# Optimization experiments

Hardware: AMD Instinct MI355X
Metric: run time of the kernel (lower is better)

The kernel has to match this reference:

```python
import jax, jax.numpy as jnp
import numpy as np

OUT_FEATURES = 4096
IN_FEATURES = 4096
NNZ = 1677722
BATCH, SEQ = 2, 2048


def setup_inputs() -> dict:
    key = jax.random.key(0)
    k1, k2, k3, k4 = jax.random.split(key, 4)
    x = jax.random.normal(k1, (BATCH, SEQ, IN_FEATURES), dtype=jnp.float32)
    data = jax.random.normal(k2, (NNZ,), dtype=jnp.float32)
    rows = jax.random.randint(k3, (NNZ,), 0, OUT_FEATURES, dtype=jnp.int32)
    cols = jax.random.randint(k4, (NNZ,), 0, IN_FEATURES, dtype=jnp.int32)
    return {"x": x, "data": data, "rows": rows, "cols": cols}


def reference(x, data, rows, cols):
    # Densify sparse weight W [out_features, in_features] from COO triples
    # (equivalent math to the CSR spmm in the original module).
    W = jnp.zeros((OUT_FEATURES, IN_FEATURES), dtype=data.dtype)
    W = W.at[rows, cols].add(data)
    # Original: (W @ x_flat.T).T reshaped -> y = x @ W^T, shape [B, S, out]
    return jnp.einsum("bsi,oi->bso", x, W)
```

## Files before the change

kernel.cpp:

```cpp
#include <hip/hip_runtime.h>
#include <stdint.h>

#define M_ROWS 4096
#define N_OUT  4096
#define K_IN   4096
#define NNZ_N  1677722
#define CAP    640

typedef __attribute__((ext_vector_type(8))) short  bf16x8_t;
typedef __attribute__((ext_vector_type(4))) float  f32x4_t;

__device__ __forceinline__ unsigned short f2bf(float f) {
    union { float f; uint32_t u; } v; v.f = f;
    uint32_t u = v.u;
    u += 0x7FFFu + ((u >> 16) & 1u);
    return (unsigned short)(u >> 16);
}

__global__ void convert_x_zero_cnt(const float4* __restrict__ x,
                                   uint4* __restrict__ xo,
                                   uint4* __restrict__ cntz) {
    int i = blockIdx.x * blockDim.x + threadIdx.x;
    if (i < 16384) {
        uint4 z; z.x = z.y = z.z = z.w = 0u;
        cntz[i] = z;
    }
    float4 a = x[2 * i], b = x[2 * i + 1];
    uint4 o;
    o.x = (uint32_t)f2bf(a.x) | ((uint32_t)f2bf(a.y) << 16);
    o.y = (uint32_t)f2bf(a.z) | ((uint32_t)f2bf(a.w) << 16);
    o.z = (uint32_t)f2bf(b.x) | ((uint32_t)f2bf(b.y) << 16);
    o.w = (uint32_t)f2bf(b.z) | ((uint32_t)f2bf(b.w) << 16);
    xo[i] = o;
}

__global__ void bin_coo(const float* __restrict__ data,
                        const int* __restrict__ rows,
                        const int* __restrict__ cols,
                        uint32_t* __restrict__ cnt,
                        uint32_t* __restrict__ bucket, int nnz) {
    int i = blockIdx.x * blockDim.x + threadIdx.x;
    if (i >= nnz) return;
    int r = rows[i];
    uint32_t slot = atomicAdd(&cnt[r << 4], 1u);
    if (slot < CAP)
        bucket[(size_t)r * CAP + slot] =
            ((uint32_t)cols[i] << 16) | (uint32_t)f2bf(data[i]);
}

__global__ __launch_bounds__(256) void accum_rows(const uint32_t* __restrict__ cnt,
                                                  const uint32_t* __restrict__ bucket,
                                                  unsigned short* __restrict__ W) {
    __shared__ float acc[K_IN];
    const int r = blockIdx.x;
    const int t = threadIdx.x;

    float4* av = (float4*)acc;
#pragma unroll
    for (int j = t; j < K_IN / 4; j += 256) av[j] = (float4){0.f, 0.f, 0.f, 0.f};
    __syncthreads();

    uint32_t n = cnt[r << 4];
    if (n > CAP) n = CAP;
    const uint32_t* b = bucket + (size_t)r * CAP;
    for (uint32_t j = t; j < n; j += 256) {
        uint32_t e = b[j];
        union { uint32_t u; float f; } v; v.u = (e & 0xFFFFu) << 16;
        atomicAdd(&acc[e >> 16], v.f);
    }
    __syncthreads();

    uint4* wv = (uint4*)(W + (size_t)r * K_IN);
#pragma unroll
    for (int j = t; j < K_IN / 8; j += 256) {
        float4 a = av[2 * j], c = av[2 * j + 1];
        uint4 o;
        o.x = (uint32_t)f2bf(a.x) | ((uint32_t)f2bf(a.y) << 16);
        o.y = (uint32_t)f2bf(a.z) | ((uint32_t)f2bf(a.w) << 16);
        o.z = (uint32_t)f2bf(c.x) | ((uint32_t)f2bf(c.y) << 16);
        o.w = (uint32_t)f2bf(c.z) | ((uint32_t)f2bf(c.w) << 16);
        wv[j] = o;
    }
}

__device__ __forceinline__ void async_ld16(const void* g, void* lds_wave_base) {
    __builtin_amdgcn_global_load_lds(
        (const __attribute__((address_space(1))) uint32_t*)g,
        (__attribute__((address_space(3))) uint32_t*)lds_wave_base,
        16, 0, 0);
}

#define STAGE_M(gbase, lbase, kt, slot) do {                                   \
    const unsigned short* g_ = (gbase) + (kt) * 64;                            \
    unsigned short*       l_ = (lbase) + (slot) * 32768;                       \
    async_ld16(g_,                  l_);                                       \
    async_ld16(g_ + 1 * 64 * K_IN,  l_ + 4096);                                \
    async_ld16(g_ + 2 * 64 * K_IN,  l_ + 8192);                                \
    async_ld16(g_ + 3 * 64 * K_IN,  l_ + 12288);                               \
} while (0)

__global__ __launch_bounds__(512, 2) void gemm_bt(const unsigned short* __restrict__ A,
                                                  const unsigned short* __restrict__ B,
                                                  float* __restrict__ C) {
    __shared__ __align__(16) unsigned short lds_[65536];

    const int t    = threadIdx.x;
    const int wave = t >> 6;
    const int lane = t & 63;
    const int wr   = wave >> 2;
    const int wc   = wave & 3;
    const int m0   = blockIdx.y * 256;
    const int n0   = blockIdx.x * 256;

    const int srow = t >> 3;
    const int sch  = ((t & 7) ^ (srow & 7)) * 8;
    const unsigned short* gA = A + (size_t)(m0 + srow) * K_IN + sch;
    const unsigned short* gB = B + (size_t)(n0 + srow) * K_IN + sch;
    unsigned short* lA = lds_ + wave * 512;
    unsigned short* lB = lds_ + 16384 + wave * 512;

    const int l15  = lane & 15;
    const int aoff = (wr * 128 + l15) * 64;
    const int boff = (wc * 64  + l15) * 64;
    const int ck0  = (((lane >> 4)    ) ^ (lane & 7)) * 8;
    const int ck1  = (((lane >> 4) | 4) ^ (lane & 7)) * 8;

    f32x4_t acc[8][4];
#pragma unroll
    for (int i = 0; i < 8; ++i)
#pragma unroll
        for (int j = 0; j < 4; ++j) acc[i][j] = (f32x4_t){0.f, 0.f, 0.f, 0.f};

    bf16x8_t af[4][2], bf0[2][2], bf1[2][2];

    STAGE_M(gA, lA, 0, 0); STAGE_M(gB, lB, 0, 0);
    STAGE_M(gA, lA, 1, 1); STAGE_M(gB, lB, 1, 1);
    asm volatile("s_waitcnt vmcnt(8)" ::: "memory");
    __builtin_amdgcn_s_barrier();

    for (int kt = 0; kt < 64; ++kt) {
        const unsigned short* pA = lds_ + (kt & 1) * 32768;
        const unsigned short* pB = pA + 16384;

#pragma unroll
        for (int im = 0; im < 4; ++im) {
            af[im][0] = *(const bf16x8_t*)(pA + aoff + im * 1024 + ck0);
            af[im][1] = *(const bf16x8_t*)(pA + aoff + im * 1024 + ck1);
        }
#pragma unroll
        for (int jn = 0; jn < 2; ++jn) {
            bf0[jn][0] = *(const bf16x8_t*)(pB + boff + jn * 1024 + ck0);
            bf0[jn][1] = *(const bf16x8_t*)(pB + boff + jn * 1024 + ck1);
        }
        __builtin_amdgcn_s_barrier();
        asm volatile("s_waitcnt lgkmcnt(0)" ::: "memory");
        __builtin_amdgcn_s_setprio(1);
#pragma unroll
        for (int im = 0; im < 4; ++im)
#pragma unroll
            for (int jn = 0; jn < 2; ++jn)
#pragma unroll
                for (int kk = 0; kk < 2; ++kk)
                    acc[im][jn] = __builtin_amdgcn_mfma_f32_16x16x32_bf16(
                        af[im][kk], bf0[jn][kk], acc[im][jn], 0, 0, 0);
        __builtin_amdgcn_s_setprio(0);
        __builtin_amdgcn_s_barrier();

#pragma unroll
        for (int jn = 0; jn < 2; ++jn) {
            bf1[jn][0] = *(const bf16x8_t*)(pB + boff + (2 + jn) * 1024 + ck0);
            bf1[jn][1] = *(const bf16x8_t*)(pB + boff + (2 + jn) * 1024 + ck1);
        }
        __builtin_amdgcn_s_barrier();
        asm volatile("s_waitcnt lgkmcnt(0)" ::: "memory");
        __builtin_amdgcn_s_setprio(1);
#pragma unroll
        for (int im = 0; im < 4; ++im)
#pragma unroll
            for (int jn = 0; jn < 2; ++jn)
#pragma unroll
                for (int kk = 0; kk < 2; ++kk)
                    acc[im][2 + jn] = __builtin_amdgcn_mfma_f32_16x16x32_bf16(
                        af[im][kk], bf1[jn][kk], acc[im][2 + jn], 0, 0, 0);
        __builtin_amdgcn_s_setprio(0);
        __builtin_amdgcn_s_barrier();

        if (kt < 62) STAGE_M(gB, lB, kt + 2, (kt & 1));
#pragma unroll
        for (int im = 0; im < 4; ++im) {
            af[im][0] = *(const bf16x8_t*)(pA + aoff + (4 + im) * 1024 + ck0);
            af[im][1] = *(const bf16x8_t*)(pA + aoff + (4 + im) * 1024 + ck1);
        }
        __builtin_amdgcn_s_barrier();
        asm volatile("s_waitcnt lgkmcnt(0)" ::: "memory");
        __builtin_amdgcn_s_setprio(1);
#pragma unroll
        for (int im = 0; im < 4; ++im)
#pragma unroll
            for (int jn = 0; jn < 2; ++jn)
#pragma unroll
                for (int kk = 0; kk < 2; ++kk)
                    acc[4 + im][jn] = __builtin_amdgcn_mfma_f32_16x16x32_bf16(
                        af[im][kk], bf0[jn][kk], acc[4 + im][jn], 0, 0, 0);
        __builtin_amdgcn_s_setprio(0);
        __builtin_amdgcn_s_barrier();

        if (kt < 62) STAGE_M(gA, lA, kt + 2, (kt & 1));
        __builtin_amdgcn_s_setprio(1);
#pragma unroll
        for (int im = 0; im < 4; ++im)
#pragma unroll
            for (int jn = 0; jn < 2; ++jn)
#pragma unroll
                for (int kk = 0; kk < 2; ++kk)
                    acc[4 + im][2 + jn] = __builtin_amdgcn_mfma_f32_16x16x32_bf16(
                        af[im][kk], bf1[jn][kk], acc[4 + im][2 + jn], 0, 0, 0);
        __builtin_amdgcn_s_setprio(0);
        if (kt < 62) {
            asm volatile("s_waitcnt vmcnt(8)" ::: "memory");
        } else {
            asm volatile("s_waitcnt vmcnt(0)" ::: "memory");
        }
        __builtin_amdgcn_s_barrier();
    }

    const int crow = m0 + wr * 128 + ((lane >> 4) << 2);
    const int ccol = n0 + wc * 64 + l15;
#pragma unroll
    for (int im = 0; im < 8; ++im)
#pragma unroll
        for (int jn = 0; jn < 4; ++jn)
#pragma unroll
            for (int r = 0; r < 4; ++r)
                C[(size_t)(crow + im * 16 + r) * N_OUT + ccol + jn * 16] =
                    acc[im][jn][r];
}

extern "C" void kernel_launch(void* const* d_in, const int* in_sizes, int n_in,
                              void* d_out, int out_size, void* d_ws, size_t ws_size,
                              hipStream_t stream) {
    const float* x    = (const float*)d_in[0];
    const float* data = (const float*)d_in[1];
    const int*   rows = (const int*)d_in[2];
    const int*   cols = (const int*)d_in[3];
    float*       out  = (float*)d_out;

    unsigned short* W_bf16 = (unsigned short*)d_ws;
    unsigned short* x_bf16 = (unsigned short*)((char*)d_ws + (32u << 20));
    uint32_t*       cnt    = (uint32_t*)((char*)d_ws + (64u << 20));
    uint32_t*       bucket = (uint32_t*)((char*)d_ws + (65u << 20));

    convert_x_zero_cnt<<<(M_ROWS * K_IN) / (8 * 256), 256, 0, stream>>>(
        (const float4*)x, (uint4*)x_bf16, (uint4*)cnt);

    bin_coo<<<(NNZ_N + 255) / 256, 256, 0, stream>>>(
        data, rows, cols, cnt, bucket, NNZ_N);

    accum_rows<<<N_OUT, 256, 0, stream>>>(cnt, bucket, W_bf16);

    dim3 grid(N_OUT / 256, M_ROWS / 256);
    gemm_bt<<<grid, 512, 0, stream>>>(x_bf16, W_bf16, out);
}
```

Baseline: 338.2 us.

## Replace global-atomic COO binning with block histogram, scan, and LDS placement

Replaces the single binning kernel, which did one global atomicAdd per nonzero on padded per-row counters, with three kernels. Each block first builds a per-chunk row histogram in shared memory, then a scan turns the histograms into per-block base offsets, and a placement pass writes entries using shared-memory atomics. The aim is to remove contention on global atomics in exchange for two extra launches, a second read of the rows array, and a histogram buffer held in global memory.

```diff
diff --git a/kernel.cpp b/kernel.cpp
--- a/kernel.cpp
+++ b/kernel.cpp
@@ -6,6 +6,8 @@
 #define K_IN   4096
 #define NNZ_N  1677722
 #define CAP    640
+#define NB     256
+#define BCHUNK 6656
 
 typedef __attribute__((ext_vector_type(8))) short  bf16x8_t;
 typedef __attribute__((ext_vector_type(4))) float  f32x4_t;
@@ -17,14 +19,8 @@
     return (unsigned short)(u >> 16);
 }
 
-__global__ void convert_x_zero_cnt(const float4* __restrict__ x,
-                                   uint4* __restrict__ xo,
-                                   uint4* __restrict__ cntz) {
+__global__ void convert_x(const float4* __restrict__ x, uint4* __restrict__ xo) {
     int i = blockIdx.x * blockDim.x + threadIdx.x;
-    if (i < 16384) {
-        uint4 z; z.x = z.y = z.z = z.w = 0u;
-        cntz[i] = z;
-    }
     float4 a = x[2 * i], b = x[2 * i + 1];
     uint4 o;
     o.x = (uint32_t)f2bf(a.x) | ((uint32_t)f2bf(a.y) << 16);
@@ -34,18 +30,65 @@
     xo[i] = o;
 }
 
-__global__ void bin_coo(const float* __restrict__ data,
-                        const int* __restrict__ rows,
-                        const int* __restrict__ cols,
-                        uint32_t* __restrict__ cnt,
-                        uint32_t* __restrict__ bucket, int nnz) {
-    int i = blockIdx.x * blockDim.x + threadIdx.x;
-    if (i >= nnz) return;
-    int r = rows[i];
-    uint32_t slot = atomicAdd(&cnt[r << 4], 1u);
-    if (slot < CAP)
-        bucket[(size_t)r * CAP + slot] =
-            ((uint32_t)cols[i] << 16) | (uint32_t)f2bf(data[i]);
+__global__ __launch_bounds__(1024) void hist_coo(const int* __restrict__ rows,
+                                                 uint32_t* __restrict__ Hist) {
+    __shared__ uint32_t h[N_OUT];
+    const int blk = blockIdx.x, t = threadIdx.x;
+    for (int j = t; j < N_OUT; j += 1024) h[j] = 0;
+    __syncthreads();
+    const int start = blk * BCHUNK;
+    const int end   = min(start + BCHUNK, NNZ_N);
+    for (int i = start + t; i < end; i += 1024)
+        atomicAdd(&h[rows[i]], 1u);
+    __syncthreads();
+    for (int j = t; j < N_OUT; j += 1024)
+        Hist[(size_t)blk * N_OUT + j] = h[j];
+}
+
+__global__ __launch_bounds__(256) void scan_hist(uint32_t* __restrict__ Hist,
+                                                 uint32_t* __restrict__ cnt) {
+    const int bin  = blockIdx.x * 4 + (threadIdx.x >> 6);
+    const int lane = threadIdx.x & 63;
+    uint32_t v[4], pre[4];
+#pragma unroll
+    for (int q = 0; q < 4; ++q)
+        v[q] = Hist[(size_t)(lane * 4 + q) * N_OUT + bin];
+    pre[0] = 0;
+#pragma unroll
+    for (int q = 1; q < 4; ++q) pre[q] = pre[q - 1] + v[q - 1];
+    uint32_t tot = pre[3] + v[3];
+    uint32_t x = tot;
+#pragma unroll
+    for (int off = 1; off < 64; off <<= 1) {
+        uint32_t y = __shfl_up(x, off);
+        if (lane >= off) x += y;
+    }
+    uint32_t excl = x - tot;
+#pragma unroll
+    for (int q = 0; q < 4; ++q)
+        Hist[(size_t)(lane * 4 + q) * N_OUT + bin] = excl + pre[q];
+    if (lane == 63) cnt[bin] = excl + tot;
+}
+
+__global__ __launch_bounds__(1024) void place_coo(const float* __restrict__ data,
+                                                  const int* __restrict__ rows,
+                                                  const int* __restrict__ cols,
+                                                  const uint32_t* __restrict__ Base,
+                                                  uint32_t* __restrict__ bucket) {
+    __shared__ uint32_t cur[N_OUT];
+    const int blk = blockIdx.x, t = threadIdx.x;
+    for (int j = t; j < N_OUT; j += 1024)
+        cur[j] = Base[(size_t)blk * N_OUT + j];
+    __syncthreads();
+    const int start = blk * BCHUNK;
+    const int end   = min(start + BCHUNK, NNZ_N);
+    for (int i = start + t; i < end; i += 1024) {
+        int r = rows[i];
+        uint32_t slot = atomicAdd(&cur[r], 1u);
+        if (slot < CAP)
+            bucket[(size_t)r * CAP + slot] =
+                ((uint32_t)cols[i] << 16) | (uint32_t)f2bf(data[i]);
+    }
 }
 
 __global__ __launch_bounds__(256) void accum_rows(const uint32_t* __restrict__ cnt,
@@ -60,7 +103,7 @@
     for (int j = t; j < K_IN / 4; j += 256) av[j] = (float4){0.f, 0.f, 0.f, 0.f};
     __syncthreads();
 
-    uint32_t n = cnt[r << 4];
+    uint32_t n = cnt[r];
     if (n > CAP) n = CAP;
     const uint32_t* b = bucket + (size_t)r * CAP;
     for (uint32_t j = t; j < n; j += 256) {
@@ -247,14 +290,18 @@
 
     unsigned short* W_bf16 = (unsigned short*)d_ws;
     unsigned short* x_bf16 = (unsigned short*)((char*)d_ws + (32u << 20));
-    uint32_t*       cnt    = (uint32_t*)((char*)d_ws + (64u << 20));
-    uint32_t*       bucket = (uint32_t*)((char*)d_ws + (65u << 20));
-
-    convert_x_zero_cnt<<<(M_ROWS * K_IN) / (8 * 256), 256, 0, stream>>>(
-        (const float4*)x, (uint4*)x_bf16, (uint4*)cnt);
-
-    bin_coo<<<(NNZ_N + 255) / 256, 256, 0, stream>>>(
-        data, rows, cols, cnt, bucket, NNZ_N);
+    uint32_t*       Hist   = (uint32_t*)((char*)d_ws + (64u << 20));
+    uint32_t*       cnt    = (uint32_t*)((char*)d_ws + (68u << 20));
+    uint32_t*       bucket = (uint32_t*)((char*)d_ws + (69u << 20));
+
+    convert_x<<<(M_ROWS * K_IN) / (8 * 256), 256, 0, stream>>>(
+        (const float4*)x, (uint4*)x_bf16);
+
+    hist_coo<<<NB, 1024, 0, stream>>>(rows, Hist);
+
+    scan_hist<<<N_OUT / 4, 256, 0, stream>>>(Hist, cnt);
+
+    place_coo<<<NB, 1024, 0, stream>>>(data, rows, cols, Hist, bucket);
 
     accum_rows<<<N_OUT, 256, 0, stream>>>(cnt, bucket, W_bf16);
 
```

After: 316.4 us. 6.4% less time.

## Replace global-atomic COO bucketing with block-local counting sort and binned accumulation

Applied to the files above, without the earlier changes.

Drops the global atomic bucketing of COO entries into fixed-capacity per-row buckets. Each of 128 blocks now counting-sorts its chunk of entries into 512 bins of 8 rows in shared memory and writes per-bin offsets. A second kernel then has each block gather its bin's segments from every chunk and accumulate 8 dense rows in 128KB of LDS before writing bf16. This removes global atomics and the silent drop of entries past the bucket cap. In exchange it uses large LDS per block, giving low occupancy, and only 128 blocks in the sort pass.

```diff
diff --git a/kernel.cpp b/kernel.cpp
--- a/kernel.cpp
+++ b/kernel.cpp
@@ -5,7 +5,9 @@
 #define N_OUT  4096
 #define K_IN   4096
 #define NNZ_N  1677722
-#define CAP    640
+#define NBLK_A 128
+#define CHUNK_A 13108
+#define NBINS  512
 
 typedef __attribute__((ext_vector_type(8))) short  bf16x8_t;
 typedef __attribute__((ext_vector_type(4))) float  f32x4_t;
@@ -17,14 +19,8 @@
     return (unsigned short)(u >> 16);
 }
 
-__global__ void convert_x_zero_cnt(const float4* __restrict__ x,
-                                   uint4* __restrict__ xo,
-                                   uint4* __restrict__ cntz) {
+__global__ void convert_x(const float4* __restrict__ x, uint4* __restrict__ xo) {
     int i = blockIdx.x * blockDim.x + threadIdx.x;
-    if (i < 16384) {
-        uint4 z; z.x = z.y = z.z = z.w = 0u;
-        cntz[i] = z;
-    }
     float4 a = x[2 * i], b = x[2 * i + 1];
     uint4 o;
     o.x = (uint32_t)f2bf(a.x) | ((uint32_t)f2bf(a.y) << 16);
@@ -34,45 +30,86 @@
     xo[i] = o;
 }
 
-__global__ void bin_coo(const float* __restrict__ data,
-                        const int* __restrict__ rows,
-                        const int* __restrict__ cols,
-                        uint32_t* __restrict__ cnt,
-                        uint32_t* __restrict__ bucket, int nnz) {
-    int i = blockIdx.x * blockDim.x + threadIdx.x;
-    if (i >= nnz) return;
-    int r = rows[i];
-    uint32_t slot = atomicAdd(&cnt[r << 4], 1u);
-    if (slot < CAP)
-        bucket[(size_t)r * CAP + slot] =
-            ((uint32_t)cols[i] << 16) | (uint32_t)f2bf(data[i]);
-}
-
-__global__ __launch_bounds__(256) void accum_rows(const uint32_t* __restrict__ cnt,
-                                                  const uint32_t* __restrict__ bucket,
+__global__ __launch_bounds__(1024) void sort_local(const float* __restrict__ data,
+                                                   const int* __restrict__ rows,
+                                                   const int* __restrict__ cols,
+                                                   uint32_t* __restrict__ run,
+                                                   uint32_t* __restrict__ Fbase) {
+    __shared__ uint32_t hist[NBINS];
+    __shared__ uint32_t basev[NBINS];
+    __shared__ uint32_t cur[NBINS];
+    __shared__ uint32_t ebuf[CHUNK_A];
+    const int blk   = blockIdx.x, t = threadIdx.x;
+    const int start = blk * CHUNK_A;
+    const int end   = min(start + CHUNK_A, NNZ_N);
+    const int nloc  = end - start;
+
+    for (int j = t; j < NBINS; j += 1024) hist[j] = 0;
+    __syncthreads();
+    for (int i = start + t; i < end; i += 1024)
+        atomicAdd(&hist[rows[i] >> 3], 1u);
+    __syncthreads();
+
+    if (t < 64) {
+        uint32_t pre[8], loc = 0;
+#pragma unroll
+        for (int q = 0; q < 8; ++q) { pre[q] = loc; loc += hist[t * 8 + q]; }
+        uint32_t x = loc;
+#pragma unroll
+        for (int off = 1; off < 64; off <<= 1) {
+            uint32_t y = __shfl_up(x, off);
+            if (t >= off) x += y;
+        }
+        uint32_t excl = x - loc;
+#pragma unroll
+        for (int q = 0; q < 8; ++q) {
+            basev[t * 8 + q] = excl + pre[q];
+            cur[t * 8 + q]   = excl + pre[q];
+        }
+    }
+    __syncthreads();
+
+    for (int i = start + t; i < end; i += 1024) {
+        int r = rows[i];
+        uint32_t slot = atomicAdd(&cur[r >> 3], 1u);
+        ebuf[slot] = ((uint32_t)(r & 7) << 28) |
+                     ((uint32_t)cols[i] << 16) | (uint32_t)f2bf(data[i]);
+    }
+    __syncthreads();
+
+    for (int j = t; j < nloc; j += 1024)
+        run[start + j] = ebuf[j];
+    if (t < NBINS) Fbase[(size_t)t * NBLK_A + blk] = basev[t];
+    if (t == 0)    Fbase[(size_t)NBINS * NBLK_A + blk] = (uint32_t)nloc;
+}
+
+__global__ __launch_bounds__(512) void accum_bins(const uint32_t* __restrict__ run,
+                                                  const uint32_t* __restrict__ Fbase,
                                                   unsigned short* __restrict__ W) {
-    __shared__ float acc[K_IN];
-    const int r = blockIdx.x;
-    const int t = threadIdx.x;
+    __shared__ float    acc[8 * K_IN];
+    __shared__ uint32_t segS[NBLK_A], segE[NBLK_A];
+    const int f = blockIdx.x, t = threadIdx.x;
 
     float4* av = (float4*)acc;
-#pragma unroll
-    for (int j = t; j < K_IN / 4; j += 256) av[j] = (float4){0.f, 0.f, 0.f, 0.f};
-    __syncthreads();
-
-    uint32_t n = cnt[r << 4];
-    if (n > CAP) n = CAP;
-    const uint32_t* b = bucket + (size_t)r * CAP;
-    for (uint32_t j = t; j < n; j += 256) {
-        uint32_t e = b[j];
-        union { uint32_t u; float f; } v; v.u = (e & 0xFFFFu) << 16;
-        atomicAdd(&acc[e >> 16], v.f);
-    }
-    __syncthreads();
-
-    uint4* wv = (uint4*)(W + (size_t)r * K_IN);
-#pragma unroll
-    for (int j = t; j < K_IN / 8; j += 256) {
+    for (int j = t; j < 8 * K_IN / 4; j += 512) av[j] = (float4){0.f, 0.f, 0.f, 0.f};
+    if (t < NBLK_A)                    segS[t]          = Fbase[(size_t)f * NBLK_A + t];
+    else if (t < 2 * NBLK_A)           segE[t - NBLK_A] = Fbase[(size_t)(f + 1) * NBLK_A + (t - NBLK_A)];
+    __syncthreads();
+
+    const int wave = t >> 6, lane = t & 63;
+    for (int blk = wave; blk < NBLK_A; blk += 8) {
+        uint32_t s = segS[blk], e = segE[blk];
+        const uint32_t* rp = run + (size_t)blk * CHUNK_A;
+        for (uint32_t j = s + lane; j < e; j += 64) {
+            uint32_t en = rp[j];
+            union { uint32_t u; float fv; } v; v.u = (en & 0xFFFFu) << 16;
+            atomicAdd(&acc[((en >> 28) & 7u) * K_IN + ((en >> 16) & 0xFFFu)], v.fv);
+        }
+    }
+    __syncthreads();
+
+    uint4* wv = (uint4*)(W + (size_t)f * 8 * K_IN);
+    for (int j = t; j < 8 * K_IN / 8; j += 512) {
         float4 a = av[2 * j], c = av[2 * j + 1];
         uint4 o;
         o.x = (uint32_t)f2bf(a.x) | ((uint32_t)f2bf(a.y) << 16);
@@ -247,16 +284,15 @@
 
     unsigned short* W_bf16 = (unsigned short*)d_ws;
     unsigned short* x_bf16 = (unsigned short*)((char*)d_ws + (32u << 20));
-    uint32_t*       cnt    = (uint32_t*)((char*)d_ws + (64u << 20));
-    uint32_t*       bucket = (uint32_t*)((char*)d_ws + (65u << 20));
-
-    convert_x_zero_cnt<<<(M_ROWS * K_IN) / (8 * 256), 256, 0, stream>>>(
-        (const float4*)x, (uint4*)x_bf16, (uint4*)cnt);
-
-    bin_coo<<<(NNZ_N + 255) / 256, 256, 0, stream>>>(
-        data, rows, cols, cnt, bucket, NNZ_N);
-
-    accum_rows<<<N_OUT, 256, 0, stream>>>(cnt, bucket, W_bf16);
+    uint32_t*       run    = (uint32_t*)((char*)d_ws + (64u << 20));
+    uint32_t*       Fbase  = (uint32_t*)((char*)d_ws + (72u << 20));
+
+    convert_x<<<(M_ROWS * K_IN) / (8 * 256), 256, 0, stream>>>(
+        (const float4*)x, (uint4*)x_bf16);
+
+    sort_local<<<NBLK_A, 1024, 0, stream>>>(data, rows, cols, run, Fbase);
+
+    accum_bins<<<NBINS, 512, 0, stream>>>(run, Fbase, W_bf16);
 
     dim3 grid(N_OUT / 256, M_ROWS / 256);
     gemm_bt<<<grid, 512, 0, stream>>>(x_bf16, W_bf16, out);
```

Result: faster. 288.1 us (-14.8%).
